# Performance work log

Measured on AMD Instinct MI355X. Metric: run time of the kernel, lower is better.

## Reference

```python
import jax, jax.numpy as jnp
import numpy as np

B, T, D, H, L = 8, 64, 128, 4, 4
G = B * T            # 512 frame-graphs
NPG = 200            # nodes per graph
N = G * NPG          # 102400 nodes
E = 8 * N            # 819200 edges
FIN, HID = 2, 64
DH = D // H
NCLS = 2


def setup_inputs():
    key = jax.random.key(0)
    ks = jax.random.split(key, 16)
    w = lambda k, s: (jax.random.normal(k, s) * 0.05).astype(jnp.float32)
    x = jax.random.normal(ks[0], (N, FIN), dtype=jnp.float32)
    g = jax.random.randint(ks[1], (E,), 0, G)
    src = (g * NPG + jax.random.randint(ks[2], (E,), 0, NPG)).astype(jnp.int32)
    dst = (g * NPG + jax.random.randint(ks[3], (E,), 0, NPG)).astype(jnp.int32)
    node_graph = (jnp.arange(N) // NPG).astype(jnp.int32)
    return dict(
        x=x, edge_src=src, edge_dst=dst, node_graph=node_graph,
        gW1=w(ks[4], (FIN, HID)), gb1=jnp.zeros((HID,), jnp.float32),
        ln1g=jnp.ones((HID,), jnp.float32), ln1b=jnp.zeros((HID,), jnp.float32),
        gW2=w(ks[5], (HID, HID)), gb2=jnp.zeros((HID,), jnp.float32),
        ln2g=jnp.ones((HID,), jnp.float32), ln2b=jnp.zeros((HID,), jnp.float32),
        gW3=w(ks[6], (HID, D)), gb3=jnp.zeros((D,), jnp.float32),
        tWqkv=w(ks[7], (L, 3 * D, D)), tbqkv=jnp.zeros((L, 3 * D), jnp.float32),
        tWo=w(ks[8], (L, D, D)), tbo=jnp.zeros((L, D), jnp.float32),
        tg1=jnp.ones((L, D), jnp.float32), tb1=jnp.zeros((L, D), jnp.float32),
        tg2=jnp.ones((L, D), jnp.float32), tb2=jnp.zeros((L, D), jnp.float32),
        tWf1=w(ks[9], (L, 4 * D, D)), tbf1=jnp.zeros((L, 4 * D), jnp.float32),
        tWf2=w(ks[10], (L, D, 4 * D)), tbf2=jnp.zeros((L, D), jnp.float32),
        hW1=w(ks[11], (D // 2, D)), hb1=jnp.zeros((D // 2,), jnp.float32),
        hW2=w(ks[12], (NCLS, D // 2)), hb2=jnp.zeros((NCLS,), jnp.float32),
    )


def _ln(x, g, b, eps=1e-5):
    m = jnp.mean(x, -1, keepdims=True)
    v = jnp.var(x, -1, keepdims=True)
    return (x - m) * jax.lax.rsqrt(v + eps) * g + b


def _forward(x, edge_src, edge_dst, node_graph, gW1, gb1, ln1g, ln1b, gW2, gb2,
             ln2g, ln2b, gW3, gb3, tWqkv, tbqkv, tWo, tbo, tg1, tb1, tg2, tb2,
             tWf1, tbf1, tWf2, tbf2, hW1, hb1, hW2, hb2):
    # --- GCN encoder (PyG GCNConv: sym-normalized A with self loops) ---
    loops = jnp.arange(N, dtype=jnp.int32)
    src = jnp.concatenate([edge_src, loops])
    dst = jnp.concatenate([edge_dst, loops])
    deg = jnp.zeros((N,), x.dtype).at[dst].add(1.0)
    dinv = jax.lax.rsqrt(deg)
    norm = (dinv[src] * dinv[dst])[:, None]

    def gcn(h, W, b):
        h = h @ W  # transform first (smaller message dim when FIN < HID)
        return jax.ops.segment_sum(h[src] * norm, dst, num_segments=N) + b

    h = _ln(jax.nn.relu(gcn(x, gW1, gb1)), ln1g, ln1b)
    h = _ln(jax.nn.relu(gcn(h, gW2, gb2)), ln2g, ln2b)
    h = gcn(h, gW3, gb3)  # (N, D)

    # per-graph mean readout (replaces the python loop in the original)
    cnt = jax.ops.segment_sum(jnp.ones((N,), h.dtype), node_graph, num_segments=G)
    emb = jax.ops.segment_sum(h, node_graph, num_segments=G) / cnt[:, None]
    seq = emb.reshape(B, T, D)

    # --- sinusoidal positional encoding ---
    pos = jnp.arange(T, dtype=jnp.float32)[:, None]
    div = jnp.exp(jnp.arange(0, D, 2, dtype=jnp.float32) * (-np.log(10000.0) / D))
    pe = jnp.zeros((T, D), jnp.float32)
    pe = pe.at[:, 0::2].set(jnp.sin(pos * div)).at[:, 1::2].set(jnp.cos(pos * div))
    seq = seq + pe

    # --- TransformerEncoder (post-norm, relu FFN, batch_first) ---
    scale = 1.0 / np.sqrt(DH)
    for l in range(L):
        qkv = seq @ tWqkv[l].T + tbqkv[l]
        q, k, v = jnp.split(qkv, 3, axis=-1)
        q = q.reshape(B, T, H, DH).transpose(0, 2, 1, 3)
        k = k.reshape(B, T, H, DH).transpose(0, 2, 1, 3)
        v = v.reshape(B, T, H, DH).transpose(0, 2, 1, 3)
        att = jax.nn.softmax(jnp.einsum('bhqd,bhkd->bhqk', q, k) * scale, axis=-1)
        a = jnp.einsum('bhqk,bhkd->bhqd', att, v).transpose(0, 2, 1, 3).reshape(B, T, D)
        seq = _ln(seq + a @ tWo[l].T + tbo[l], tg1[l], tb1[l])
        f = jax.nn.relu(seq @ tWf1[l].T + tbf1[l]) @ tWf2[l].T + tbf2[l]
        seq = _ln(seq + f, tg2[l], tb2[l])

    pooled = jnp.mean(seq, axis=1)  # mask=None path -> plain temporal mean
    return jax.nn.relu(pooled @ hW1.T + hb1) @ hW2.T + hb2  # (B, NCLS)


def reference(x, edge_src, edge_dst, node_graph, gW1, gb1, ln1g, ln1b, gW2, gb2,
              ln2g, ln2b, gW3, gb3, tWqkv, tbqkv, tWo, tbo, tg1, tb1, tg2, tb2,
              tWf1, tbf1, tWf2, tbf2, hW1, hb1, hW2, hb2):
    return _forward(x, edge_src, edge_dst, node_graph, gW1, gb1, ln1g, ln1b,
                    gW2, gb2, ln2g, ln2b, gW3, gb3, tWqkv, tbqkv, tWo, tbo,
                    tg1, tb1, tg2, tb2, tWf1, tbf1, tWf2, tbf2, hW1, hb1, hW2, hb2)
```

## Files before the change

kernel.cpp:

```cpp
#include <hip/hip_runtime.h>

#define NN   102400
#define EE   819200
#define GG   512
#define NPG  200
#define DD   128
#define TT   64
#define BB   8
#define LL   4
#define NB_A   320
#define ECH_A  2560
#define SCAP 2560
#define NSLOT 16
#define CHK  25

typedef unsigned int uint;

static __device__ __forceinline__ void wave_sum64_2(float& a, float& b) {
#pragma unroll
    for (int off = 32; off > 0; off >>= 1) {
        a += __shfl_xor(a, off, 64);
        b += __shfl_xor(b, off, 64);
    }
}


__global__ __launch_bounds__(256) void k_a1(const int* __restrict__ src,
                                            int* __restrict__ hist) {
    __shared__ int h[GG];
    int tid = threadIdx.x;
    h[tid] = 0; h[tid + 256] = 0;
    __syncthreads();
    int base = blockIdx.x * ECH_A;
#pragma unroll
    for (int it = 0; it < ECH_A / 256; ++it)
        atomicAdd(&h[src[base + it * 256 + tid] / NPG], 1);
    __syncthreads();
    hist[blockIdx.x * GG + tid] = h[tid];
    hist[blockIdx.x * GG + tid + 256] = h[tid + 256];
}

__global__ __launch_bounds__(512) void k_a2(const int* __restrict__ hist,
                                            int* __restrict__ off2,
                                            int* __restrict__ goff) {
    __shared__ int sm[GG];
    int g = threadIdx.x;
    int s = 0;
    for (int b = 0; b < NB_A; ++b) s += hist[b * GG + g];
    sm[g] = s;
    __syncthreads();
    for (int d = 1; d < GG; d <<= 1) {
        int v = (g >= d) ? sm[g - d] : 0;
        __syncthreads();
        sm[g] += v;
        __syncthreads();
    }
    int base = sm[g] - s;
    goff[g] = base;
    if (g == GG - 1) goff[GG] = sm[g];
    int run = base;
    for (int b = 0; b < NB_A; ++b) {
        off2[b * GG + g] = run;
        run += hist[b * GG + g];
    }
}

__global__ __launch_bounds__(256) void k_a3(const int* __restrict__ src,
                                            const int* __restrict__ dst,
                                            const int* __restrict__ off2,
                                            uint* __restrict__ gpack) {
    __shared__ int cur[GG];
    int tid = threadIdx.x;
    cur[tid] = off2[blockIdx.x * GG + tid];
    cur[tid + 256] = off2[blockIdx.x * GG + tid + 256];
    __syncthreads();
    int base = blockIdx.x * ECH_A;
#pragma unroll
    for (int it = 0; it < ECH_A / 256; ++it) {
        int e = base + it * 256 + tid;
        int s = src[e], d = dst[e];
        int g = s / NPG;
        int pos = atomicAdd(&cur[g], 1);
        gpack[pos] = ((uint)(s - g * NPG) << 8) | (uint)(d - g * NPG);
    }
}

__global__ __launch_bounds__(256) void k_bsort(
    const float* __restrict__ x, const int* __restrict__ goff,
    const uint* __restrict__ gpack, const float* __restrict__ W1,
    const float* __restrict__ gb1, const float* __restrict__ lng,
    const float* __restrict__ lnb, uint2* __restrict__ slots,
    uint2* __restrict__ ovf, int* __restrict__ ovfcnt,
    float* __restrict__ wgtv, float* __restrict__ hout) {
    int g = ((blockIdx.x & 7) << 6) | (blockIdx.x >> 3);
    __shared__ float2 xs[NPG];
    __shared__ float2 aggl[NPG];
    __shared__ int cnt2[NPG];
    __shared__ int lnoff[NPG + 1];
    __shared__ int cur[NPG];
    __shared__ float rsq[NPG];
    __shared__ float cwl[NPG];
    __shared__ uint srec[SCAP];
    __shared__ int sm[256];
    __shared__ uint2 ovfl[128];
    __shared__ int ovfcur;
    int tid = threadIdx.x;
    int base = goff[g], E = goff[g + 1] - base;
    const float2* x2 = (const float2*)x;
    if (tid < NPG) { xs[tid] = x2[g * NPG + tid]; cnt2[tid] = 0; cwl[tid] = 0.f; }
    if (tid == 0) ovfcur = 0;
    __syncthreads();
    for (int i = tid; i < E; i += 256) atomicAdd(&cnt2[gpack[base + i] & 255u], 1);
    __syncthreads();
    int c = (tid < NPG) ? cnt2[tid] : 0;
    sm[tid] = c;
    __syncthreads();
    for (int d = 1; d < 256; d <<= 1) {
        int v = (tid >= d) ? sm[tid - d] : 0;
        __syncthreads();
        sm[tid] += v;
        __syncthreads();
    }
    if (tid < NPG) {
        lnoff[tid] = sm[tid] - c;
        cur[tid] = sm[tid] - c;
        rsq[tid] = rsqrtf((float)(c + 1));
    }
    if (tid == 0) lnoff[NPG] = E;
    __syncthreads();
    for (int i = tid; i < E; i += 256) {
        uint r = gpack[base + i];
        int pos = atomicAdd(&cur[r & 255u], 1);
        srec[pos] = r;
    }
    __syncthreads();
    for (int i = tid; i < E; i += 256) {
        uint r = srec[i];
        atomicAdd(&cwl[r >> 8], rsq[r >> 8] * rsq[r & 255u]);
    }
    __syncthreads();
    {
        uint2* sbase = &slots[(size_t)g * NPG * NSLOT];
        for (int li = tid; li < NPG * NSLOT; li += 256) {
            int n = li >> 4, s = li & 15;
            int e0 = lnoff[n];
            int En = lnoff[n + 1] - e0;
            float rd = rsq[n];
            uint2 v;
            if (s == 0) {
                v = make_uint2((uint)(g * NPG + n), __float_as_uint(rd * rd));
            } else if (s - 1 < En) {
                uint r = srec[e0 + s - 1];
                int ls = (int)(r >> 8);
                v = make_uint2((uint)(g * NPG + ls), __float_as_uint(rsq[ls] * rd));
            } else {
                v = make_uint2((uint)(g * NPG + n), 0u);
            }
            sbase[li] = v;
        }
    }
    if (tid < NPG) {
        float rd = rsq[tid];
        float dv = rd * rd;
        float ax = xs[tid].x * dv, ay = xs[tid].y * dv;
        int e0 = lnoff[tid], e1 = lnoff[tid + 1];
        for (int e = e0; e < e1; ++e) {
            uint r = srec[e];
            int ls = (int)(r >> 8);
            float w = rsq[ls] * rd;
            ax += xs[ls].x * w;
            ay += xs[ls].y * w;
        }
        for (int e = e0 + NSLOT - 1; e < e1; ++e) {
            uint r = srec[e];
            int ls = (int)(r >> 8);
            int p = atomicAdd(&ovfcur, 1);
            if (p < 128)
                ovfl[p] = make_uint2(((uint)tid << 17) | (uint)(g * NPG + ls),
                                     __float_as_uint(rsq[ls] * rd));
        }
        aggl[tid] = make_float2(ax, ay);
        wgtv[g * NPG + tid] = cwl[tid] + dv;
    }
    __syncthreads();
    int nov = ovfcur < 128 ? ovfcur : 128;
    if (tid == 0) ovfcnt[g] = nov;
    if (tid < nov) ovf[g * 128 + tid] = ovfl[tid];
    int lane = tid & 63, wid = tid >> 6;
    float w0 = W1[lane], w1 = W1[64 + lane];
    float gbj = gb1[lane], lgj = lng[lane], lbj = lnb[lane];
    for (int i = wid; i < NPG; i += 4) {
        float2 a = aggl[i];
        float u = fmaxf(a.x * w0 + a.y * w1 + gbj, 0.f);
        float s2 = u, q2 = u * u;
        wave_sum64_2(s2, q2);
        float mean = s2 * (1.f / 64.f);
        float var = q2 * (1.f / 64.f) - mean * mean;
        hout[(size_t)(g * NPG + i) * 64 + lane] = (u - mean) * rsqrtf(var + 1e-5f) * lgj + lbj;
    }
}


__global__ __launch_bounds__(256, 4) void k_agg_lin_ln(
    const float* __restrict__ t, const float* __restrict__ W,
    const float* __restrict__ gb, const float* __restrict__ lng,
    const float* __restrict__ lnb, const uint2* __restrict__ slots,
    const uint2* __restrict__ ovf, const int* __restrict__ ovfcnt,
    float* __restrict__ hout) {
    int c = ((blockIdx.x & 7) << 9) | (blockIdx.x >> 3);
    int n0 = c * CHK;
    int g = c >> 3, lbase = (c & 7) * CHK;
    __shared__ float hs[CHK][64];
    __shared__ uint2 slt[CHK][NSLOT];
    int tid = threadIdx.x, lane = tid & 63, wid = tid >> 6;
    int grp = lane >> 4, fq = lane & 15;
    {
        const float4* s4 = (const float4*)&slots[(size_t)n0 * NSLOT];
        float4* d4 = (float4*)slt;
        for (int i = tid; i < CHK * NSLOT / 2; i += 256) d4[i] = s4[i];
    }
    __syncthreads();
    for (int i = wid; i < CHK; i += 4) {
        float4 acc = make_float4(0.f, 0.f, 0.f, 0.f);
#pragma unroll
        for (int r = 0; r < 4; ++r) {
            uint2 s = slt[i][r * 4 + grp];
            float w = __uint_as_float(s.y);
            float4 tv = *(const float4*)&t[(size_t)s.x * 64 + fq * 4];
            acc.x += tv.x * w; acc.y += tv.y * w;
            acc.z += tv.z * w; acc.w += tv.w * w;
        }
        acc.x += __shfl_xor(acc.x, 16); acc.y += __shfl_xor(acc.y, 16);
        acc.z += __shfl_xor(acc.z, 16); acc.w += __shfl_xor(acc.w, 16);
        acc.x += __shfl_xor(acc.x, 32); acc.y += __shfl_xor(acc.y, 32);
        acc.z += __shfl_xor(acc.z, 32); acc.w += __shfl_xor(acc.w, 32);
        if (grp == 0) *(float4*)&hs[i][fq * 4] = acc;
    }
    __syncthreads();
    int nov = ovfcnt[g];
    if (nov && wid == 0) {
        for (int k = 0; k < nov; ++k) {
            uint2 r = ovf[g * 128 + k];
            int ld = r.x >> 17;
            if (ld >= lbase && ld < lbase + CHK)
                hs[ld - lbase][lane] +=
                    t[(size_t)(r.x & 0x1FFFFu) * 64 + lane] * __uint_as_float(r.y);
        }
    }
    __syncthreads();
    float wreg[64];
#pragma unroll
    for (int k = 0; k < 64; ++k) wreg[k] = W[k * 64 + lane];
    float gbj = gb[lane], lgj = lng[lane], lbj = lnb[lane];
    for (int i = wid; i < CHK; i += 4) {
        const float4* hrow = (const float4*)&hs[i][0];
        float a0 = 0.f, a1 = 0.f;
#pragma unroll
        for (int k4 = 0; k4 < 16; k4 += 2) {
            float4 h0 = hrow[k4], h1 = hrow[k4 + 1];
            a0 += h0.x * wreg[4 * k4] + h0.y * wreg[4 * k4 + 1] +
                  h0.z * wreg[4 * k4 + 2] + h0.w * wreg[4 * k4 + 3];
            a1 += h1.x * wreg[4 * k4 + 4] + h1.y * wreg[4 * k4 + 5] +
                  h1.z * wreg[4 * k4 + 6] + h1.w * wreg[4 * k4 + 7];
        }
        float u = fmaxf(a0 + a1 + gbj, 0.f);
        float s = u, q = u * u;
        wave_sum64_2(s, q);
        float mean = s * (1.f / 64.f);
        float var = q * (1.f / 64.f) - mean * mean;
        hout[(size_t)(n0 + i) * 64 + lane] = (u - mean) * rsqrtf(var + 1e-5f) * lgj + lbj;
    }
}

__global__ __launch_bounds__(256) void k_wpool_emb(
    const float* __restrict__ h2, const float* __restrict__ wgtv,
    const float* __restrict__ W3, const float* __restrict__ b3,
    float* __restrict__ seq) {
    int g = ((blockIdx.x & 7) << 6) | (blockIdx.x >> 3);
    int n0 = g * NPG;
    __shared__ float wgt[NPG];
    __shared__ float red[16][64];
    __shared__ float ps[64];
    int tid = threadIdx.x, lane = tid & 63, w = tid >> 6;
    int grp = lane >> 4, fq = lane & 15;
    for (int i = tid; i < NPG; i += 256) wgt[i] = wgtv[n0 + i];
    __syncthreads();
    float4 acc = make_float4(0.f, 0.f, 0.f, 0.f);
    for (int row = w * 4 + grp; row < NPG; row += 16) {
        float4 v = *(const float4*)&h2[(size_t)(n0 + row) * 64 + fq * 4];
        float wg = wgt[row];
        acc.x += v.x * wg; acc.y += v.y * wg; acc.z += v.z * wg; acc.w += v.w * wg;
    }
    *(float4*)&red[w * 4 + grp][fq * 4] = acc;
    __syncthreads();
    if (tid < 64) {
        float s = 0.f;
#pragma unroll
        for (int k = 0; k < 16; ++k) s += red[k][tid];
        ps[tid] = s * (1.f / NPG);
    }
    __syncthreads();
    if (tid < 128) {
        int d = tid;
        float a = b3[d];
#pragma unroll 8
        for (int k = 0; k < 64; ++k) a += ps[k] * W3[k * DD + d];
        float freq = expf((float)(d & ~1) * (-9.210340371976184f / 128.f));
        float ang = (float)(g & (TT - 1)) * freq;
        a += (d & 1) ? cosf(ang) : sinf(ang);
        seq[(size_t)g * DD + d] = a;
    }
}


__global__ __launch_bounds__(512) void k_qkv_attn(
    const float* __restrict__ seq, const float* __restrict__ Wqkv,
    const float* __restrict__ bqkv, float* __restrict__ abuf) {
    int b = blockIdx.x >> 2, h = blockIdx.x & 3;
    __shared__ float seqs[64][132];
    __shared__ float Qs[64][36], Ks[64][36], Vs[64][36];
    __shared__ float Ss[64][68];
    int tid = threadIdx.x;
    for (int i = tid; i < 64 * 32; i += 512) {
        int r = i >> 5, c = i & 31;
        float4 v = *(const float4*)&seq[(size_t)(b * 64 + r) * DD + c * 4];
        *(float4*)&seqs[r][c * 4] = v;
    }
    __syncthreads();
    {
        int r = tid & 63, jg = tid >> 6;
        float acc[12];
        int wrow[12];
#pragma unroll
        for (int i = 0; i < 12; ++i) {
            int jj = jg * 12 + i;
            int row = (jj < 32) ? (h * 32 + jj)
                    : (jj < 64) ? (128 + h * 32 + jj - 32)
                                : (256 + h * 32 + jj - 64);
            wrow[i] = row;
            acc[i] = bqkv[row];
        }
        for (int kc = 0; kc < 8; ++kc) {
            float4 s0 = *(const float4*)&seqs[r][kc * 16 + 0];
            float4 s1 = *(const float4*)&seqs[r][kc * 16 + 4];
            float4 s2 = *(const float4*)&seqs[r][kc * 16 + 8];
            float4 s3 = *(const float4*)&seqs[r][kc * 16 + 12];
#pragma unroll
            for (int i = 0; i < 12; ++i) {
                const float4* wp = (const float4*)&Wqkv[(size_t)wrow[i] * DD + kc * 16];
                float4 w0 = wp[0], w1 = wp[1], w2 = wp[2], w3 = wp[3];
                acc[i] += s0.x * w0.x + s0.y * w0.y + s0.z * w0.z + s0.w * w0.w +
                          s1.x * w1.x + s1.y * w1.y + s1.z * w1.z + s1.w * w1.w +
                          s2.x * w2.x + s2.y * w2.y + s2.z * w2.z + s2.w * w2.w +
                          s3.x * w3.x + s3.y * w3.y + s3.z * w3.z + s3.w * w3.w;
            }
        }
#pragma unroll
        for (int i = 0; i < 12; ++i) {
            int jj = jg * 12 + i;
            if (jj < 32) Qs[r][jj] = acc[i];
            else if (jj < 64) Ks[r][jj - 32] = acc[i];
            else Vs[r][jj - 64] = acc[i];
        }
    }
    __syncthreads();
    int q = tid >> 3, kg = tid & 7;
    const float scale = 0.17677669529663687f;
    float p[8];
    float mx = -1e30f;
#pragma unroll
    for (int kk = 0; kk < 8; ++kk) {
        int k = kg * 8 + kk;
        float a = 0.f;
#pragma unroll
        for (int dq = 0; dq < 8; ++dq) {
            float4 qv = *(const float4*)&Qs[q][dq * 4];
            float4 kv = *(const float4*)&Ks[k][dq * 4];
            a += qv.x * kv.x + qv.y * kv.y + qv.z * kv.z + qv.w * kv.w;
        }
        p[kk] = a * scale;
        mx = fmaxf(mx, p[kk]);
    }
    mx = fmaxf(mx, __shfl_xor(mx, 1));
    mx = fmaxf(mx, __shfl_xor(mx, 2));
    mx = fmaxf(mx, __shfl_xor(mx, 4));
    float ssum = 0.f;
#pragma unroll
    for (int kk = 0; kk < 8; ++kk) {
        p[kk] = expf(p[kk] - mx);
        ssum += p[kk];
    }
    ssum += __shfl_xor(ssum, 1);
    ssum += __shfl_xor(ssum, 2);
    ssum += __shfl_xor(ssum, 4);
    float inv = 1.f / ssum;
#pragma unroll
    for (int kk = 0; kk < 8; ++kk) Ss[q][kg * 8 + kk] = p[kk] * inv;
    __syncthreads();
    float4 o = make_float4(0.f, 0.f, 0.f, 0.f);
    for (int k = 0; k < 64; ++k) {
        float pw = Ss[q][k];
        float4 v = *(const float4*)&Vs[k][kg * 4];
        o.x += pw * v.x; o.y += pw * v.y; o.z += pw * v.z; o.w += pw * v.w;
    }
    *(float4*)&abuf[(size_t)(b * 64 + q) * DD + h * 32 + kg * 4] = o;
}

__global__ __launch_bounds__(256) void k_post(
    const float* __restrict__ abuf, const float* __restrict__ Wo,
    const float* __restrict__ bo, const float* __restrict__ g1,
    const float* __restrict__ bl1, const float* __restrict__ Wf1,
    const float* __restrict__ bf1, const float* __restrict__ Wf2,
    const float* __restrict__ bf2, const float* __restrict__ g2,
    const float* __restrict__ bl2, float* __restrict__ seq) {
    int m0 = blockIdx.x * 2, tid = threadIdx.x;
    __shared__ float arow[2][128];
    __shared__ float srow[2][128];
    __shared__ float f1[2][512];
    __shared__ float pf[2][128];
    __shared__ float sred[4][2];
    __shared__ float sred2[2][4];
    int rr = tid >> 7, d0 = tid & 127;
    arow[rr][d0] = abuf[(size_t)(m0 + rr) * DD + d0];
    __syncthreads();
    {
        float acc = bo[d0];
        const float4* wr = (const float4*)&Wo[(size_t)d0 * DD];
        const float4* ar = (const float4*)arow[rr];
#pragma unroll
        for (int k = 0; k < 32; ++k) {
            float4 w = wr[k], a = ar[k];
            acc += a.x * w.x + a.y * w.y + a.z * w.z + a.w * w.w;
        }
        float u = seq[(size_t)(m0 + rr) * DD + d0] + acc;
        float s = u, q = u * u;
        wave_sum64_2(s, q);
        int wv = tid >> 6;
        if ((tid & 63) == 0) { sred[wv][0] = s; sred[wv][1] = q; }
        __syncthreads();
        int wp = rr * 2;
        s = sred[wp][0] + sred[wp + 1][0];
        q = sred[wp][1] + sred[wp + 1][1];
        float mean = s * (1.f / 128.f);
        float var = q * (1.f / 128.f) - mean * mean;
        float rstd = rsqrtf(var + 1e-5f);
        srow[rr][d0] = (u - mean) * rstd * g1[d0] + bl1[d0];
    }
    __syncthreads();
    const float4* s0 = (const float4*)srow[0];
    const float4* s1 = (const float4*)srow[1];
#pragma unroll
    for (int rep = 0; rep < 2; ++rep) {
        int o = tid + rep * 256;
        float bv = bf1[o];
        float a0 = bv, a1 = bv;
        const float4* wr = (const float4*)&Wf1[(size_t)o * DD];
#pragma unroll
        for (int k = 0; k < 32; ++k) {
            float4 w = wr[k];
            float4 x0 = s0[k], x1 = s1[k];
            a0 += x0.x * w.x + x0.y * w.y + x0.z * w.z + x0.w * w.w;
            a1 += x1.x * w.x + x1.y * w.y + x1.z * w.z + x1.w * w.w;
        }
        f1[0][o] = fmaxf(a0, 0.f);
        f1[1][o] = fmaxf(a1, 0.f);
    }
    __syncthreads();
    int d = tid & 127, half = tid >> 7;
    float b0 = half ? 0.f : bf2[d];
    float a0 = b0, a1 = b0;
    const float4* wr2 = (const float4*)&Wf2[(size_t)d * 512 + half * 256];
    const float4* f10 = (const float4*)&f1[0][half * 256];
    const float4* f11 = (const float4*)&f1[1][half * 256];
#pragma unroll
    for (int k = 0; k < 64; ++k) {
        float4 w = wr2[k];
        float4 x0 = f10[k], x1 = f11[k];
        a0 += x0.x * w.x + x0.y * w.y + x0.z * w.z + x0.w * w.w;
        a1 += x1.x * w.x + x1.y * w.y + x1.z * w.z + x1.w * w.w;
    }
    if (half) { pf[0][d] = a0; pf[1][d] = a1; }
    __syncthreads();
    if (half == 0) {
        float u0 = srow[0][d] + a0 + pf[0][d];
        float u1 = srow[1][d] + a1 + pf[1][d];
        float s0_ = u0, q0_ = u0 * u0, s1_ = u1, q1_ = u1 * u1;
        wave_sum64_2(s0_, q0_);
        wave_sum64_2(s1_, q1_);
        int w_ = d >> 6;
        if ((d & 63) == 0) {
            sred2[w_][0] = s0_; sred2[w_][1] = q0_;
            sred2[w_][2] = s1_; sred2[w_][3] = q1_;
        }
        __syncthreads();
        float S0 = sred2[0][0] + sred2[1][0], Q0 = sred2[0][1] + sred2[1][1];
        float S1 = sred2[0][2] + sred2[1][2], Q1 = sred2[0][3] + sred2[1][3];
        float mean0 = S0 * (1.f / 128.f);
        float var0 = Q0 * (1.f / 128.f) - mean0 * mean0;
        float rstd0 = rsqrtf(var0 + 1e-5f);
        float mean1 = S1 * (1.f / 128.f);
        float var1 = Q1 * (1.f / 128.f) - mean1 * mean1;
        float rstd1 = rsqrtf(var1 + 1e-5f);
        seq[(size_t)m0 * DD + d] = (u0 - mean0) * rstd0 * g2[d] + bl2[d];
        seq[(size_t)(m0 + 1) * DD + d] = (u1 - mean1) * rstd1 * g2[d] + bl2[d];
    } else {
        __syncthreads();
    }
}

__global__ __launch_bounds__(128) void k_head(
    const float* __restrict__ seq, const float* __restrict__ W1,
    const float* __restrict__ b1, const float* __restrict__ W2,
    const float* __restrict__ b2, float* __restrict__ out) {
    int b = blockIdx.x, t = threadIdx.x;
    __shared__ float pooled[DD];
    __shared__ float hid[64];
    float s = 0.f;
    for (int i = 0; i < TT; ++i) s += seq[(size_t)(b * TT + i) * DD + t];
    pooled[t] = s * (1.f / TT);
    __syncthreads();
    if (t < 64) {
        float a = b1[t];
        const float* wr = W1 + t * DD;
        for (int k = 0; k < DD; ++k) a += pooled[k] * wr[k];
        hid[t] = fmaxf(a, 0.f);
    }
    __syncthreads();
    if (t < 2) {
        float a = b2[t];
        const float* wr = W2 + t * 64;
        for (int k = 0; k < 64; ++k) a += hid[k] * wr[k];
        out[b * 2 + t] = a;
    }
}


extern "C" void kernel_launch(void* const* d_in, const int* in_sizes, int n_in,
                              void* d_out, int out_size, void* d_ws, size_t ws_size,
                              hipStream_t stream) {
    const float* x     = (const float*)d_in[0];
    const int*   esrc  = (const int*)d_in[1];
    const int*   edst  = (const int*)d_in[2];
    const float* gW1   = (const float*)d_in[4];
    const float* gb1   = (const float*)d_in[5];
    const float* ln1g  = (const float*)d_in[6];
    const float* ln1b  = (const float*)d_in[7];
    const float* gW2   = (const float*)d_in[8];
    const float* gb2   = (const float*)d_in[9];
    const float* ln2g  = (const float*)d_in[10];
    const float* ln2b  = (const float*)d_in[11];
    const float* gW3   = (const float*)d_in[12];
    const float* gb3   = (const float*)d_in[13];
    const float* tWqkv = (const float*)d_in[14];
    const float* tbqkv = (const float*)d_in[15];
    const float* tWo   = (const float*)d_in[16];
    const float* tbo   = (const float*)d_in[17];
    const float* tg1   = (const float*)d_in[18];
    const float* tb1   = (const float*)d_in[19];
    const float* tg2   = (const float*)d_in[20];
    const float* tb2   = (const float*)d_in[21];
    const float* tWf1  = (const float*)d_in[22];
    const float* tbf1  = (const float*)d_in[23];
    const float* tWf2  = (const float*)d_in[24];
    const float* tbf2  = (const float*)d_in[25];
    const float* hW1   = (const float*)d_in[26];
    const float* hb1   = (const float*)d_in[27];
    const float* hW2   = (const float*)d_in[28];
    const float* hb2   = (const float*)d_in[29];
    float* out = (float*)d_out;

    int*   hist   = (int*)d_ws;
    int*   off2   = hist + NB_A * GG;
    int*   goff   = off2 + NB_A * GG;
    uint*  gpack  = (uint*)(goff + 516);
    uint2* slots  = (uint2*)(gpack + EE);
    uint2* ovf    = slots + (size_t)NN * NSLOT;
    int*   ovfcnt = (int*)(ovf + GG * 128);
    float* wgtv   = (float*)(ovfcnt + GG);
    float* bufA = wgtv + NN;
    float* bufB = bufA + (size_t)NN * 64;
    float* seq  = bufB + (size_t)NN * 64;
    float* abuf = seq + GG * DD;

    k_a1<<<NB_A, 256, 0, stream>>>(esrc, hist);
    k_a2<<<1, 512, 0, stream>>>(hist, off2, goff);
    k_a3<<<NB_A, 256, 0, stream>>>(esrc, edst, off2, gpack);
    k_bsort<<<GG, 256, 0, stream>>>(x, goff, gpack, gW1, gb1, ln1g, ln1b,
                                    slots, ovf, ovfcnt, wgtv, bufA);

    k_agg_lin_ln<<<NN / CHK, 256, 0, stream>>>(bufA, gW2, gb2, ln2g, ln2b,
                                               slots, ovf, ovfcnt, bufB);
    k_wpool_emb<<<GG, 256, 0, stream>>>(bufB, wgtv, gW3, gb3, seq);

    for (int l = 0; l < LL; l++) {
        k_qkv_attn<<<BB * 4, 512, 0, stream>>>(
            seq, tWqkv + (size_t)l * 384 * 128, tbqkv + l * 384, abuf);
        k_post<<<GG / 2, 256, 0, stream>>>(
            abuf, tWo + (size_t)l * 128 * 128, tbo + l * 128,
            tg1 + l * 128, tb1 + l * 128,
            tWf1 + (size_t)l * 512 * 128, tbf1 + l * 512,
            tWf2 + (size_t)l * 128 * 512, tbf2 + l * 128,
            tg2 + l * 128, tb2 + l * 128, seq);
    }

    k_head<<<BB, DD, 0, stream>>>(seq, hW1, hb1, hW2, hb2, out);
}
```

Before: 385.5 us.

## Fuse weighted pooling into aggregation kernel and parallelize histogram prefix scan

The single-block scan over per-block edge histograms is split into three kernels: a parallel per-graph column reduction, a small scan, and a wave-parallel per-graph scan that writes the per-block offsets. The second GCN layer kernel now accumulates the weighted node pooling directly into a per-graph buffer with atomics, so the 102400x64 intermediate is no longer written and re-read. The chunk size is doubled to 50 nodes per block. A separate small kernel then applies the embedding and positional encoding. The changes add a memset, extra launches and float atomic ordering nondeterminism, and the launch-bounds occupancy hint is dropped.

```diff
diff --git a/kernel.cpp b/kernel.cpp
--- a/kernel.cpp
+++ b/kernel.cpp
@@ -12,7 +12,7 @@
 #define ECH_A  2560
 #define SCAP 2560
 #define NSLOT 16
-#define CHK  25
+#define CHK  50
 
 typedef unsigned int uint;
 
@@ -40,14 +40,23 @@
     hist[blockIdx.x * GG + tid + 256] = h[tid + 256];
 }
 
-__global__ __launch_bounds__(512) void k_a2(const int* __restrict__ hist,
-                                            int* __restrict__ off2,
-                                            int* __restrict__ goff) {
+__global__ __launch_bounds__(64) void k_a2a(const int* __restrict__ hist,
+                                            int* __restrict__ gcnt) {
+    int g = blockIdx.x, lane = threadIdx.x;
+    int s = 0;
+#pragma unroll
+    for (int i = 0; i < NB_A / 64; ++i) s += hist[(i * 64 + lane) * GG + g];
+#pragma unroll
+    for (int off = 32; off > 0; off >>= 1) s += __shfl_xor(s, off, 64);
+    if (lane == 0) gcnt[g] = s;
+}
+
+__global__ __launch_bounds__(512) void k_a2b(const int* __restrict__ gcnt,
+                                             int* __restrict__ goff) {
     __shared__ int sm[GG];
     int g = threadIdx.x;
-    int s = 0;
-    for (int b = 0; b < NB_A; ++b) s += hist[b * GG + g];
-    sm[g] = s;
+    int c = gcnt[g];
+    sm[g] = c;
     __syncthreads();
     for (int d = 1; d < GG; d <<= 1) {
         int v = (g >= d) ? sm[g - d] : 0;
@@ -55,13 +64,28 @@
         sm[g] += v;
         __syncthreads();
     }
-    int base = sm[g] - s;
-    goff[g] = base;
+    goff[g] = sm[g] - c;
     if (g == GG - 1) goff[GG] = sm[g];
-    int run = base;
-    for (int b = 0; b < NB_A; ++b) {
-        off2[b * GG + g] = run;
-        run += hist[b * GG + g];
+}
+
+__global__ __launch_bounds__(512) void k_a2c(const int* __restrict__ hist,
+                                             const int* __restrict__ goff,
+                                             int* __restrict__ off2) {
+    int g = blockIdx.x * 8 + (threadIdx.x >> 6);
+    int lane = threadIdx.x & 63;
+    int running = goff[g];
+#pragma unroll
+    for (int cchunk = 0; cchunk < NB_A / 64; ++cchunk) {
+        int b = cchunk * 64 + lane;
+        int v = hist[b * GG + g];
+        int s = v;
+#pragma unroll
+        for (int off = 1; off < 64; off <<= 1) {
+            int t_ = __shfl_up(s, off, 64);
+            if (lane >= off) s += t_;
+        }
+        off2[b * GG + g] = running + s - v;
+        running += __shfl(s, 63, 64);
     }
 }
 
@@ -201,17 +225,19 @@
 }
 
 
-__global__ __launch_bounds__(256, 4) void k_agg_lin_ln(
+__global__ __launch_bounds__(256) void k_agg_lin_pool(
     const float* __restrict__ t, const float* __restrict__ W,
     const float* __restrict__ gb, const float* __restrict__ lng,
     const float* __restrict__ lnb, const uint2* __restrict__ slots,
     const uint2* __restrict__ ovf, const int* __restrict__ ovfcnt,
-    float* __restrict__ hout) {
-    int c = ((blockIdx.x & 7) << 9) | (blockIdx.x >> 3);
+    const float* __restrict__ wgtv, float* __restrict__ pooled) {
+    int c = ((blockIdx.x & 7) << 8) | (blockIdx.x >> 3);
     int n0 = c * CHK;
-    int g = c >> 3, lbase = (c & 7) * CHK;
+    int g = c >> 2, lbase = (c & 3) * CHK;
     __shared__ float hs[CHK][64];
     __shared__ uint2 slt[CHK][NSLOT];
+    __shared__ float wgt[CHK];
+    __shared__ float red[4][64];
     int tid = threadIdx.x, lane = tid & 63, wid = tid >> 6;
     int grp = lane >> 4, fq = lane & 15;
     {
@@ -219,6 +245,7 @@
         float4* d4 = (float4*)slt;
         for (int i = tid; i < CHK * NSLOT / 2; i += 256) d4[i] = s4[i];
     }
+    if (tid < CHK) wgt[tid] = wgtv[n0 + tid];
     __syncthreads();
     for (int i = wid; i < CHK; i += 4) {
         float4 acc = make_float4(0.f, 0.f, 0.f, 0.f);
@@ -252,6 +279,7 @@
 #pragma unroll
     for (int k = 0; k < 64; ++k) wreg[k] = W[k * 64 + lane];
     float gbj = gb[lane], lgj = lng[lane], lbj = lnb[lane];
+    float psum = 0.f;
     for (int i = wid; i < CHK; i += 4) {
         const float4* hrow = (const float4*)&hs[i][0];
         float a0 = 0.f, a1 = 0.f;
@@ -268,48 +296,30 @@
         wave_sum64_2(s, q);
         float mean = s * (1.f / 64.f);
         float var = q * (1.f / 64.f) - mean * mean;
-        hout[(size_t)(n0 + i) * 64 + lane] = (u - mean) * rsqrtf(var + 1e-5f) * lgj + lbj;
-    }
-}
-
-__global__ __launch_bounds__(256) void k_wpool_emb(
-    const float* __restrict__ h2, const float* __restrict__ wgtv,
-    const float* __restrict__ W3, const float* __restrict__ b3,
-    float* __restrict__ seq) {
-    int g = ((blockIdx.x & 7) << 6) | (blockIdx.x >> 3);
-    int n0 = g * NPG;
-    __shared__ float wgt[NPG];
-    __shared__ float red[16][64];
+        float h = (u - mean) * rsqrtf(var + 1e-5f) * lgj + lbj;
+        psum += h * wgt[i];
+    }
+    red[wid][lane] = psum;
+    __syncthreads();
+    if (tid < 64)
+        atomicAdd(&pooled[g * 64 + tid],
+                  red[0][tid] + red[1][tid] + red[2][tid] + red[3][tid]);
+}
+
+__global__ __launch_bounds__(128) void k_emb(
+    const float* __restrict__ pooled, const float* __restrict__ W3,
+    const float* __restrict__ b3, float* __restrict__ seq) {
+    int g = blockIdx.x, d = threadIdx.x;
     __shared__ float ps[64];
-    int tid = threadIdx.x, lane = tid & 63, w = tid >> 6;
-    int grp = lane >> 4, fq = lane & 15;
-    for (int i = tid; i < NPG; i += 256) wgt[i] = wgtv[n0 + i];
-    __syncthreads();
-    float4 acc = make_float4(0.f, 0.f, 0.f, 0.f);
-    for (int row = w * 4 + grp; row < NPG; row += 16) {
-        float4 v = *(const float4*)&h2[(size_t)(n0 + row) * 64 + fq * 4];
-        float wg = wgt[row];
-        acc.x += v.x * wg; acc.y += v.y * wg; acc.z += v.z * wg; acc.w += v.w * wg;
-    }
-    *(float4*)&red[w * 4 + grp][fq * 4] = acc;
-    __syncthreads();
-    if (tid < 64) {
-        float s = 0.f;
-#pragma unroll
-        for (int k = 0; k < 16; ++k) s += red[k][tid];
-        ps[tid] = s * (1.f / NPG);
-    }
-    __syncthreads();
-    if (tid < 128) {
-        int d = tid;
-        float a = b3[d];
+    if (d < 64) ps[d] = pooled[g * 64 + d] * (1.f / NPG);
+    __syncthreads();
+    float a = b3[d];
 #pragma unroll 8
-        for (int k = 0; k < 64; ++k) a += ps[k] * W3[k * DD + d];
-        float freq = expf((float)(d & ~1) * (-9.210340371976184f / 128.f));
-        float ang = (float)(g & (TT - 1)) * freq;
-        a += (d & 1) ? cosf(ang) : sinf(ang);
-        seq[(size_t)g * DD + d] = a;
-    }
+    for (int k = 0; k < 64; ++k) a += ps[k] * W3[k * DD + d];
+    float freq = expf((float)(d & ~1) * (-9.210340371976184f / 128.f));
+    float ang = (float)(g & (TT - 1)) * freq;
+    a += (d & 1) ? cosf(ang) : sinf(ang);
+    seq[(size_t)g * DD + d] = a;
 }
 
 
@@ -571,26 +581,30 @@
 
     int*   hist   = (int*)d_ws;
     int*   off2   = hist + NB_A * GG;
-    int*   goff   = off2 + NB_A * GG;
+    int*   gcnt   = off2 + NB_A * GG;
+    int*   goff   = gcnt + GG;
     uint*  gpack  = (uint*)(goff + 516);
     uint2* slots  = (uint2*)(gpack + EE);
     uint2* ovf    = slots + (size_t)NN * NSLOT;
     int*   ovfcnt = (int*)(ovf + GG * 128);
     float* wgtv   = (float*)(ovfcnt + GG);
-    float* bufA = wgtv + NN;
-    float* bufB = bufA + (size_t)NN * 64;
-    float* seq  = bufB + (size_t)NN * 64;
+    float* pooled = wgtv + NN;
+    float* bufA = pooled + GG * 64;
+    float* seq  = bufA + (size_t)NN * 64;
     float* abuf = seq + GG * DD;
 
+    hipMemsetAsync(pooled, 0, GG * 64 * sizeof(float), stream);
     k_a1<<<NB_A, 256, 0, stream>>>(esrc, hist);
-    k_a2<<<1, 512, 0, stream>>>(hist, off2, goff);
+    k_a2a<<<GG, 64, 0, stream>>>(hist, gcnt);
+    k_a2b<<<1, 512, 0, stream>>>(gcnt, goff);
+    k_a2c<<<64, 512, 0, stream>>>(hist, goff, off2);
     k_a3<<<NB_A, 256, 0, stream>>>(esrc, edst, off2, gpack);
     k_bsort<<<GG, 256, 0, stream>>>(x, goff, gpack, gW1, gb1, ln1g, ln1b,
                                     slots, ovf, ovfcnt, wgtv, bufA);
 
-    k_agg_lin_ln<<<NN / CHK, 256, 0, stream>>>(bufA, gW2, gb2, ln2g, ln2b,
-                                               slots, ovf, ovfcnt, bufB);
-    k_wpool_emb<<<GG, 256, 0, stream>>>(bufB, wgtv, gW3, gb3, seq);
+    k_agg_lin_pool<<<NN / CHK, 256, 0, stream>>>(bufA, gW2, gb2, ln2g, ln2b,
+                                                 slots, ovf, ovfcnt, wgtv, pooled);
+    k_emb<<<GG, DD, 0, stream>>>(pooled, gW3, gb3, seq);
 
     for (int l = 0; l < LL; l++) {
         k_qkv_attn<<<BB * 4, 512, 0, stream>>>(
```

Measured after the change: 368.6 us. 1.05x faster.
